# Optimization experiments

Hardware: AMD Instinct MI355X
Metric: run time of the kernel (lower is better)

Reference implementation:

```python
import jax, jax.numpy as jnp
import numpy as np

B, S, HID = 2, 2048, 2304
NH, NKV, HD = 8, 4, 256
GROUPS = NH // NKV
SCALE = 256 ** -0.5          # query_pre_attn_scalar ** -0.5
SOFTCAP = 50.0               # attn_logit_softcapping
ROPE_THETA = 10000.0


def setup_inputs() -> dict:
    key = jax.random.key(0)
    ks = jax.random.split(key, 5)
    return {
        "hidden_states": jax.random.normal(ks[0], (B, S, HID), dtype=jnp.float32),
        "wq": jax.random.normal(ks[1], (HID, NH * HD), dtype=jnp.float32) * 0.02,
        "wk": jax.random.normal(ks[2], (HID, NKV * HD), dtype=jnp.float32) * 0.02,
        "wv": jax.random.normal(ks[3], (HID, NKV * HD), dtype=jnp.float32) * 0.02,
        "wo": jax.random.normal(ks[4], (NH * HD, HID), dtype=jnp.float32) * 0.02,
    }


def _rope_cos_sin(seq_len, dim, dtype):
    inv_freq = 1.0 / (ROPE_THETA ** (jnp.arange(0, dim, 2, dtype=jnp.float32) / dim))
    pos = jnp.arange(seq_len, dtype=jnp.float32)
    freqs = pos[:, None] * inv_freq[None, :]            # [S, HD/2]
    emb = jnp.concatenate([freqs, freqs], axis=-1)      # [S, HD]
    return jnp.cos(emb).astype(dtype), jnp.sin(emb).astype(dtype)


def _rotate_half(x):
    x1, x2 = jnp.split(x, 2, axis=-1)
    return jnp.concatenate([-x2, x1], axis=-1)


def reference(hidden_states, wq, wk, wv, wo):
    b, s, _ = hidden_states.shape
    # projections -> [B, H, S, D]
    q = (hidden_states @ wq).reshape(b, s, NH, HD).transpose(0, 2, 1, 3)
    k = (hidden_states @ wk).reshape(b, s, NKV, HD).transpose(0, 2, 1, 3)
    v = (hidden_states @ wv).reshape(b, s, NKV, HD).transpose(0, 2, 1, 3)

    cos, sin = _rope_cos_sin(s, HD, q.dtype)            # [S, HD]
    q = q * cos + _rotate_half(q) * sin
    k = k * cos + _rotate_half(k) * sin

    # GQA repeat_kv
    k = jnp.repeat(k, GROUPS, axis=1)                   # [B, NH, S, D]
    v = jnp.repeat(v, GROUPS, axis=1)

    scores = jnp.einsum("bhqd,bhkd->bhqk", q, k) * SCALE
    # tanh logit softcapping
    scores = SOFTCAP * jnp.tanh(scores / SOFTCAP)
    # causal additive mask
    neg = jnp.finfo(scores.dtype).min
    causal = jnp.tril(jnp.ones((s, s), dtype=bool))
    scores = jnp.where(causal[None, None], scores, neg)

    probs = jax.nn.softmax(scores, axis=-1).astype(q.dtype)
    attn = jnp.einsum("bhqk,bhkd->bhqd", probs, v)      # [B, NH, S, D]
    attn = attn.transpose(0, 2, 1, 3).reshape(b, s, NH * HD)
    return attn @ wo
```

## Files before the change

### kernel.cpp

```cpp
#include <hip/hip_runtime.h>
#include <hip/hip_bf16.h>

typedef __attribute__((ext_vector_type(8))) short short8;
typedef __attribute__((ext_vector_type(4))) float f32x4;
typedef __attribute__((ext_vector_type(4))) unsigned short ushort4_;
typedef __attribute__((ext_vector_type(2))) unsigned long ulong2_;

__device__ __forceinline__ unsigned short f2bf(float f) {
  unsigned u = __builtin_bit_cast(unsigned, f);
  u += 0x7fff + ((u >> 16) & 1);
  return (unsigned short)(u >> 16);
}

__global__ void sincos_kernel(float2* __restrict__ table) {
  int idx = blockIdx.x * 256 + threadIdx.x;
  int s = idx >> 7, i = idx & 127;
  float inv = exp2f(-(float)i * (13.287712379549449f / 128.0f));
  float ang = (float)s * inv;
  table[idx] = make_float2(cosf(ang), sinf(ang));
}

__global__ void convert_x_kernel(const float* __restrict__ in, unsigned short* __restrict__ out, int n4) {
  int idx = blockIdx.x * 256 + threadIdx.x;
  if (idx >= n4) return;
  float4 v = ((const float4*)in)[idx];
  ushort4_ o = { f2bf(v.x), f2bf(v.y), f2bf(v.z), f2bf(v.w) };
  *(ushort4_*)(out + (size_t)idx * 4) = o;
}

__global__ __launch_bounds__(256) void wtrans_kernel(const float* __restrict__ in,
                                                     unsigned short* __restrict__ out,
                                                     int R, int C) {
  __shared__ float t[32][33];
  int tx = threadIdx.x & 31, ty = threadIdx.x >> 5;
  int r0 = blockIdx.y * 32, c0 = blockIdx.x * 32;
#pragma unroll
  for (int k = 0; k < 4; ++k) t[ty + k * 8][tx] = in[(size_t)(r0 + ty + k * 8) * C + c0 + tx];
  __syncthreads();
#pragma unroll
  for (int k = 0; k < 4; ++k) out[(size_t)(c0 + ty + k * 8) * R + r0 + tx] = f2bf(t[tx][ty + k * 8]);
}

__global__ __launch_bounds__(256) void vtrans_kernel(const float* __restrict__ qkv,
                                                     unsigned short* __restrict__ Vt) {
  __shared__ float t[32][33];
  int z = blockIdx.z; int b = z >> 2, hk = z & 3;
  const float* in = qkv + (size_t)b * 2048 * 4096 + 3072 + hk * 256;
  unsigned short* out = Vt + (size_t)z * 256 * 2048;
  int tx = threadIdx.x & 31, ty = threadIdx.x >> 5;
  int r0 = blockIdx.y * 32, c0 = blockIdx.x * 32;
#pragma unroll
  for (int k = 0; k < 4; ++k) t[ty + k * 8][tx] = in[(size_t)(r0 + ty + k * 8) * 4096 + c0 + tx];
  __syncthreads();
#pragma unroll
  for (int k = 0; k < 4; ++k) out[(size_t)(c0 + ty + k * 8) * 2048 + r0 + tx] = f2bf(t[tx][ty + k * 8]);
}

__global__ void rope_kernel(const float* __restrict__ qkv, const float2* __restrict__ table,
                            unsigned short* __restrict__ Qb, unsigned short* __restrict__ Kb) {
  int idx = blockIdx.x * 256 + threadIdx.x;
  int i = idx & 127;
  int rest = idx >> 7;
  int h12 = rest % 12;
  int rest2 = rest / 12;
  int s = rest2 & 2047;
  int b = rest2 >> 11;
  float2 cs = table[(s << 7) + i];
  size_t row = (size_t)b * 2048 + s;
  size_t col; unsigned short* out;
  if (h12 < 8) { col = (size_t)h12 * 256; out = Qb + (((size_t)(b * 8 + h12) * 2048 + s) << 8); }
  else { int hk = h12 - 8; col = 2048 + (size_t)hk * 256; out = Kb + (((size_t)(b * 4 + hk) * 2048 + s) << 8); }
  float x1 = qkv[row * 4096 + col + i];
  float x2 = qkv[row * 4096 + col + 128 + i];
  out[i]       = f2bf(x1 * cs.x - x2 * cs.y);
  out[128 + i] = f2bf(x2 * cs.x + x1 * cs.y);
}

__global__ __launch_bounds__(256) void gemm_bt_kernel(const unsigned short* __restrict__ A,
                                                      const unsigned short* __restrict__ Bt,
                                                      float* __restrict__ C, int M, int N, int K) {
  __shared__ unsigned short sA[128 * 32];
  __shared__ unsigned short sB[128 * 32];
  int tid = threadIdx.x;
  int lane = tid & 63, w = tid >> 6;
  int wr = w >> 1, wc = w & 1;
  int lr = lane & 15, lg = lane >> 4;
  long m0 = (long)blockIdx.x * 128, n0 = (long)blockIdx.y * 128;
  f32x4 acc[4][4] = {};
  int nkt = K >> 5;
  for (int kt = 0; kt < nkt; ++kt) {
    __syncthreads();
    long k0 = (long)kt * 32;
#pragma unroll
    for (int p = 0; p < 2; ++p) {
      int c = p * 256 + tid;
      int row = c >> 2, colb = (c & 3) * 8;
      int dst = (c * 8) ^ ((row & 3) << 3);
      *(ulong2_*)&sA[dst] = *(const ulong2_*)&A[(m0 + row) * K + k0 + colb];
      *(ulong2_*)&sB[dst] = *(const ulong2_*)&Bt[(n0 + row) * K + k0 + colb];
    }
    __syncthreads();
    short8 af[4], bg[4];
#pragma unroll
    for (int mi = 0; mi < 4; ++mi) {
      int row = wr * 64 + mi * 16 + lr;
      int e = (row * 32 + lg * 8) ^ ((row & 3) << 3);
      af[mi] = *(const short8*)&sA[e];
    }
#pragma unroll
    for (int ni = 0; ni < 4; ++ni) {
      int row = wc * 64 + ni * 16 + lr;
      int e = (row * 32 + lg * 8) ^ ((row & 3) << 3);
      bg[ni] = *(const short8*)&sB[e];
    }
#pragma unroll
    for (int mi = 0; mi < 4; ++mi)
#pragma unroll
      for (int ni = 0; ni < 4; ++ni)
        acc[mi][ni] = __builtin_amdgcn_mfma_f32_16x16x32_bf16(af[mi], bg[ni], acc[mi][ni], 0, 0, 0);
  }
#pragma unroll
  for (int mi = 0; mi < 4; ++mi)
#pragma unroll
    for (int ni = 0; ni < 4; ++ni) {
      long r = m0 + wr * 64 + mi * 16 + lg * 4;
      long cc = n0 + wc * 64 + ni * 16 + lr;
#pragma unroll
      for (int i = 0; i < 4; ++i)
        C[(r + i) * N + cc] = acc[mi][ni][i];
    }
}

__global__ __launch_bounds__(256) void attn_kernel(const unsigned short* __restrict__ Qb,
                                                   const unsigned short* __restrict__ Kb,
                                                   const unsigned short* __restrict__ Vt,
                                                   unsigned short* __restrict__ attnb) {
  __shared__ unsigned short sK[64 * 256];
  __shared__ unsigned short sV[256 * 64];
  __shared__ unsigned short sP[4][16 * 64];
  int qt = blockIdx.x, bh = blockIdx.y;
  int b = bh >> 3, h = bh & 7, hk = h >> 1;
  const unsigned short* Qh = Qb + ((size_t)(b * 8 + h) << 19);
  const unsigned short* Kh = Kb + ((size_t)(b * 4 + hk) << 19);
  const unsigned short* Vh = Vt + ((size_t)(b * 4 + hk) << 19);
  int tid = threadIdx.x, w = tid >> 6, lane = tid & 63;
  int lr = lane & 15, lg = lane >> 4;

  short8 qf[8];
  int qrow = qt * 64 + w * 16 + lr;
#pragma unroll
  for (int kc = 0; kc < 8; ++kc)
    qf[kc] = *(const short8*)&Qh[(size_t)qrow * 256 + kc * 32 + lg * 8];

  f32x4 acc[16] = {};
  float m_i[4], l_i[4];
#pragma unroll
  for (int i = 0; i < 4; ++i) { m_i[i] = -1e30f; l_i[i] = 0.f; }
  int qbase = qt * 64 + w * 16 + lg * 4;

  for (int kt2 = 0; kt2 <= qt; ++kt2) {
    __syncthreads();
#pragma unroll
    for (int p = 0; p < 8; ++p) {
      int c = p * 256 + tid;
      {
        int row = c >> 5;
        int dste = (c * 8) ^ ((row & 7) << 3);
        *(ulong2_*)&sK[dste] = *(const ulong2_*)&Kh[(size_t)kt2 * 16384 + (size_t)c * 8];
      }
      {
        int r = c >> 3, ccn = c & 7;
        int dste = (r * 64 + ccn * 8) ^ ((r & 7) << 3);
        *(ulong2_*)&sV[dste] = *(const ulong2_*)&Vh[(size_t)r * 2048 + kt2 * 64 + ccn * 8];
      }
    }
    __syncthreads();

    f32x4 sf[4] = {};
#pragma unroll
    for (int nf = 0; nf < 4; ++nf) {
#pragma unroll
      for (int kc = 0; kc < 8; ++kc) {
        int row = nf * 16 + lr;
        int e = (row * 256 + kc * 32 + lg * 8) ^ ((row & 7) << 3);
        short8 kfr = *(const short8*)&sK[e];
        sf[nf] = __builtin_amdgcn_mfma_f32_16x16x32_bf16(qf[kc], kfr, sf[nf], 0, 0, 0);
      }
    }

    float pv[4][4];
    float pmax[4], psum[4];
#pragma unroll
    for (int i = 0; i < 4; ++i) pmax[i] = -1e30f;
    int kcol = kt2 * 64 + lr;
#pragma unroll
    for (int nf = 0; nf < 4; ++nf)
#pragma unroll
      for (int i = 0; i < 4; ++i) {
        float x = sf[nf][i] * (0.0625f / 50.0f);
        x = fminf(fmaxf(x, -10.f), 10.f);
        float e2 = __expf(2.f * x);
        float sc = 50.f * ((e2 - 1.f) * __builtin_amdgcn_rcpf(e2 + 1.f));
        bool masked = (kcol + nf * 16) > (qbase + i);
        sc = masked ? -1e30f : sc;
        pv[nf][i] = sc;
        pmax[i] = fmaxf(pmax[i], sc);
      }
#pragma unroll
    for (int d = 1; d < 16; d <<= 1)
#pragma unroll
      for (int i = 0; i < 4; ++i)
        pmax[i] = fmaxf(pmax[i], __shfl_xor(pmax[i], d));
    float scale_f[4];
#pragma unroll
    for (int i = 0; i < 4; ++i) {
      float m_new = fmaxf(m_i[i], pmax[i]);
      scale_f[i] = __expf(m_i[i] - m_new);
      m_i[i] = m_new;
      psum[i] = 0.f;
    }
#pragma unroll
    for (int nf = 0; nf < 4; ++nf)
#pragma unroll
      for (int i = 0; i < 4; ++i) {
        float p = __expf(pv[nf][i] - m_i[i]);
        pv[nf][i] = p;
        psum[i] += p;
      }
#pragma unroll
    for (int d = 1; d < 16; d <<= 1)
#pragma unroll
      for (int i = 0; i < 4; ++i)
        psum[i] += __shfl_xor(psum[i], d);
#pragma unroll
    for (int i = 0; i < 4; ++i)
      l_i[i] = l_i[i] * scale_f[i] + psum[i];
#pragma unroll
    for (int df = 0; df < 16; ++df)
#pragma unroll
      for (int i = 0; i < 4; ++i)
        acc[df][i] *= scale_f[i];

#pragma unroll
    for (int nf = 0; nf < 4; ++nf)
#pragma unroll
      for (int i = 0; i < 4; ++i)
        sP[w][(lg * 4 + i) * 64 + nf * 16 + lr] = f2bf(pv[nf][i]);
    asm volatile("s_waitcnt lgkmcnt(0)" ::: "memory");
    short8 pa[2];
#pragma unroll
    for (int kc2 = 0; kc2 < 2; ++kc2)
      pa[kc2] = *(const short8*)&sP[w][lr * 64 + kc2 * 32 + lg * 8];

#pragma unroll
    for (int df = 0; df < 16; ++df)
#pragma unroll
      for (int kc2 = 0; kc2 < 2; ++kc2) {
        int row = df * 16 + lr;
        int e = (row * 64 + kc2 * 32 + lg * 8) ^ ((row & 7) << 3);
        short8 vfr = *(const short8*)&sV[e];
        acc[df] = __builtin_amdgcn_mfma_f32_16x16x32_bf16(pa[kc2], vfr, acc[df], 0, 0, 0);
      }
  }

  float invl[4];
#pragma unroll
  for (int i = 0; i < 4; ++i) invl[i] = 1.0f / l_i[i];
  size_t mrow = (size_t)b * 2048 + qt * 64 + w * 16 + lg * 4;
#pragma unroll
  for (int df = 0; df < 16; ++df)
#pragma unroll
    for (int i = 0; i < 4; ++i)
      attnb[(mrow + i) * 2048 + h * 256 + df * 16 + lr] = f2bf(acc[df][i] * invl[i]);
}

extern "C" void kernel_launch(void* const* d_in, const int* in_sizes, int n_in,
                              void* d_out, int out_size, void* d_ws, size_t ws_size,
                              hipStream_t stream) {
  const float* hidden = (const float*)d_in[0];
  const float* wq = (const float*)d_in[1];
  const float* wk = (const float*)d_in[2];
  const float* wv = (const float*)d_in[3];
  const float* wo = (const float*)d_in[4];
  float* out = (float*)d_out;

  char* ws = (char*)d_ws;
  size_t off = 0;
  auto alloc = [&](size_t bytes) { void* p = ws + off; off += (bytes + 255) & ~255ULL; return p; };
  float2* table = (float2*)alloc((size_t)2048 * 128 * sizeof(float2));
  unsigned short* Xb    = (unsigned short*)alloc((size_t)4096 * 2304 * 2);
  unsigned short* WallT = (unsigned short*)alloc((size_t)4096 * 2304 * 2);
  unsigned short* WoT   = (unsigned short*)alloc((size_t)2304 * 2048 * 2);
  float*          QKV   = (float*)alloc((size_t)4096 * 4096 * 4);
  unsigned short* Qb    = (unsigned short*)alloc((size_t)2 * 8 * 2048 * 256 * 2);
  unsigned short* Kb    = (unsigned short*)alloc((size_t)2 * 4 * 2048 * 256 * 2);
  unsigned short* Vt    = (unsigned short*)alloc((size_t)2 * 4 * 2048 * 256 * 2);
  unsigned short* attnb = (unsigned short*)QKV;

  sincos_kernel<<<1024, 256, 0, stream>>>(table);
  convert_x_kernel<<<9216, 256, 0, stream>>>(hidden, Xb, 2359296);
  wtrans_kernel<<<dim3(64, 72), 256, 0, stream>>>(wq, WallT, 2304, 2048);
  wtrans_kernel<<<dim3(32, 72), 256, 0, stream>>>(wk, WallT + (size_t)2048 * 2304, 2304, 1024);
  wtrans_kernel<<<dim3(32, 72), 256, 0, stream>>>(wv, WallT + (size_t)3072 * 2304, 2304, 1024);
  wtrans_kernel<<<dim3(72, 64), 256, 0, stream>>>(wo, WoT, 2048, 2304);
  gemm_bt_kernel<<<dim3(32, 32), 256, 0, stream>>>(Xb, WallT, QKV, 4096, 4096, 2304);
  rope_kernel<<<24576, 256, 0, stream>>>(QKV, table, Qb, Kb);
  vtrans_kernel<<<dim3(8, 64, 8), 256, 0, stream>>>(QKV, Vt);
  attn_kernel<<<dim3(32, 16), 256, 0, stream>>>(Qb, Kb, Vt, attnb);
  gemm_bt_kernel<<<dim3(32, 18), 256, 0, stream>>>(attnb, WoT, out, 4096, 2304, 2048);
}
```

Measured before the change: 576.6 us.

## Split attention KV range across two blocks with combine pass; use LDS direct loads in GEMM

The attention kernel now splits each query tile's causal KV range into two halves handled by separate blocks, with the longest tiles scheduled first. Each half writes unnormalized fp32 partial outputs and per-row max/sum, and a new combine kernel merges them into bf16. This raises the block count and evens out causal load imbalance, at the cost of extra fp32 traffic and another launch. Separately, the GEMM switches to global_load_lds direct-to-LDS loads and drops the XOR swizzle, which may add LDS bank conflicts on fragment reads.

```diff
diff --git a/kernel.cpp b/kernel.cpp
--- a/kernel.cpp
+++ b/kernel.cpp
@@ -10,6 +10,11 @@
   unsigned u = __builtin_bit_cast(unsigned, f);
   u += 0x7fff + ((u >> 16) & 1);
   return (unsigned short)(u >> 16);
+}
+
+__device__ __forceinline__ void gload16(const unsigned short* g, unsigned short* l) {
+  __builtin_amdgcn_global_load_lds((const __attribute__((address_space(1))) unsigned int*)g,
+                                   (__attribute__((address_space(3))) unsigned int*)l, 16, 0, 0);
 }
 
 __global__ void sincos_kernel(float2* __restrict__ table) {
@@ -95,24 +100,17 @@
     for (int p = 0; p < 2; ++p) {
       int c = p * 256 + tid;
       int row = c >> 2, colb = (c & 3) * 8;
-      int dst = (c * 8) ^ ((row & 3) << 3);
-      *(ulong2_*)&sA[dst] = *(const ulong2_*)&A[(m0 + row) * K + k0 + colb];
-      *(ulong2_*)&sB[dst] = *(const ulong2_*)&Bt[(n0 + row) * K + k0 + colb];
+      gload16(&A[(m0 + row) * K + k0 + colb], &sA[c * 8]);
+      gload16(&Bt[(n0 + row) * K + k0 + colb], &sB[c * 8]);
     }
     __syncthreads();
     short8 af[4], bg[4];
 #pragma unroll
-    for (int mi = 0; mi < 4; ++mi) {
-      int row = wr * 64 + mi * 16 + lr;
-      int e = (row * 32 + lg * 8) ^ ((row & 3) << 3);
-      af[mi] = *(const short8*)&sA[e];
-    }
-#pragma unroll
-    for (int ni = 0; ni < 4; ++ni) {
-      int row = wc * 64 + ni * 16 + lr;
-      int e = (row * 32 + lg * 8) ^ ((row & 3) << 3);
-      bg[ni] = *(const short8*)&sB[e];
-    }
+    for (int mi = 0; mi < 4; ++mi)
+      af[mi] = *(const short8*)&sA[(wr * 64 + mi * 16 + lr) * 32 + lg * 8];
+#pragma unroll
+    for (int ni = 0; ni < 4; ++ni)
+      bg[ni] = *(const short8*)&sB[(wc * 64 + ni * 16 + lr) * 32 + lg * 8];
 #pragma unroll
     for (int mi = 0; mi < 4; ++mi)
 #pragma unroll
@@ -134,11 +132,15 @@
 __global__ __launch_bounds__(256) void attn_kernel(const unsigned short* __restrict__ Qb,
                                                    const unsigned short* __restrict__ Kb,
                                                    const unsigned short* __restrict__ Vt,
-                                                   unsigned short* __restrict__ attnb) {
+                                                   float* __restrict__ Op,
+                                                   float* __restrict__ ml) {
   __shared__ unsigned short sK[64 * 256];
   __shared__ unsigned short sV[256 * 64];
   __shared__ unsigned short sP[4][16 * 64];
-  int qt = blockIdx.x, bh = blockIdx.y;
+  int bh = blockIdx.x, y = blockIdx.y;
+  int qt = 31 - (y >> 1), s = y & 1;
+  int ntile = qt + 1, half = (ntile + 1) >> 1;
+  int k0t = s ? half : 0, k1t = s ? ntile : half;
   int b = bh >> 3, h = bh & 7, hk = h >> 1;
   const unsigned short* Qh = Qb + ((size_t)(b * 8 + h) << 19);
   const unsigned short* Kh = Kb + ((size_t)(b * 4 + hk) << 19);
@@ -158,7 +160,7 @@
   for (int i = 0; i < 4; ++i) { m_i[i] = -1e30f; l_i[i] = 0.f; }
   int qbase = qt * 64 + w * 16 + lg * 4;
 
-  for (int kt2 = 0; kt2 <= qt; ++kt2) {
+  for (int kt2 = k0t; kt2 < k1t; ++kt2) {
     __syncthreads();
 #pragma unroll
     for (int p = 0; p < 8; ++p) {
@@ -263,15 +265,41 @@
       }
   }
 
-  float invl[4];
-#pragma unroll
-  for (int i = 0; i < 4; ++i) invl[i] = 1.0f / l_i[i];
-  size_t mrow = (size_t)b * 2048 + qt * 64 + w * 16 + lg * 4;
+  size_t orow = (size_t)bh * 2048 + qbase;
 #pragma unroll
   for (int df = 0; df < 16; ++df)
 #pragma unroll
     for (int i = 0; i < 4; ++i)
-      attnb[(mrow + i) * 2048 + h * 256 + df * 16 + lr] = f2bf(acc[df][i] * invl[i]);
+      Op[(((orow + i) * 2 + s) << 8) + df * 16 + lr] = acc[df][i];
+  if (lr == 0) {
+#pragma unroll
+    for (int i = 0; i < 4; ++i) {
+      ml[(orow + i) * 4 + s * 2]     = m_i[i];
+      ml[(orow + i) * 4 + s * 2 + 1] = l_i[i];
+    }
+  }
+}
+
+__global__ void combine_kernel(const float* __restrict__ Op, const float* __restrict__ ml,
+                               unsigned short* __restrict__ attnb) {
+  int idx = blockIdx.x * 256 + threadIdx.x;
+  int c4 = idx & 63;
+  int rest = idx >> 6;
+  const float* mlp = ml + (size_t)rest * 4;
+  float m0 = mlp[0], l0 = mlp[1], m1 = mlp[2], l1 = mlp[3];
+  float m = fmaxf(m0, m1);
+  float w0 = __expf(m0 - m), w1 = __expf(m1 - m);
+  float inv = 1.0f / (l0 * w0 + l1 * w1);
+  const float4 o0 = *(const float4*)&Op[(((size_t)rest * 2 + 0) << 8) + c4 * 4];
+  const float4 o1 = *(const float4*)&Op[(((size_t)rest * 2 + 1) << 8) + c4 * 4];
+  int row = rest & 2047, bh = rest >> 11;
+  int b = bh >> 3, h = bh & 7;
+  ushort4_ o;
+  o.x = f2bf((o0.x * w0 + o1.x * w1) * inv);
+  o.y = f2bf((o0.y * w0 + o1.y * w1) * inv);
+  o.z = f2bf((o0.z * w0 + o1.z * w1) * inv);
+  o.w = f2bf((o0.w * w0 + o1.w * w1) * inv);
+  *(ushort4_*)&attnb[((size_t)(b * 2048 + row)) * 2048 + h * 256 + c4 * 4] = o;
 }
 
 extern "C" void kernel_launch(void* const* d_in, const int* in_sizes, int n_in,
@@ -295,7 +323,9 @@
   unsigned short* Qb    = (unsigned short*)alloc((size_t)2 * 8 * 2048 * 256 * 2);
   unsigned short* Kb    = (unsigned short*)alloc((size_t)2 * 4 * 2048 * 256 * 2);
   unsigned short* Vt    = (unsigned short*)alloc((size_t)2 * 4 * 2048 * 256 * 2);
-  unsigned short* attnb = (unsigned short*)QKV;
+  float*          Op    = QKV;
+  float*          mlbuf = (float*)table;
+  unsigned short* attnb = Xb;
 
   sincos_kernel<<<1024, 256, 0, stream>>>(table);
   convert_x_kernel<<<9216, 256, 0, stream>>>(hidden, Xb, 2359296);
@@ -306,6 +336,7 @@
   gemm_bt_kernel<<<dim3(32, 32), 256, 0, stream>>>(Xb, WallT, QKV, 4096, 4096, 2304);
   rope_kernel<<<24576, 256, 0, stream>>>(QKV, table, Qb, Kb);
   vtrans_kernel<<<dim3(8, 64, 8), 256, 0, stream>>>(QKV, Vt);
-  attn_kernel<<<dim3(32, 16), 256, 0, stream>>>(Qb, Kb, Vt, attnb);
+  attn_kernel<<<dim3(16, 64), 256, 0, stream>>>(Qb, Kb, Vt, Op, mlbuf);
+  combine_kernel<<<8192, 256, 0, stream>>>(Op, mlbuf, attnb);
   gemm_bt_kernel<<<dim3(32, 18), 256, 0, stream>>>(attnb, WoT, out, 4096, 2304, 2048);
 }
```

Result: faster. 470.2 us (-18.4%).
